# Performance work log

Hardware: AMD Instinct MI355X
Metric: run time of the kernel (lower is better)

The kernel has to match this reference:

```python
import jax, jax.numpy as jnp
import numpy as np

# t2t / fold constants (FuseFormer defaults)
K = 7      # kernel size
S = 3      # stride
P = 3      # padding
H, W = 60, 108          # fold output_size
LH = (H + 2 * P - K) // S + 1   # 20
LW = (W + 2 * P - K) // S + 1   # 36
NVECS = LH * LW                 # 720


def _patch_indices():
    # row[k, i] = k + S*i : row coordinate in the padded image for kernel offset k, window i
    row = jnp.arange(K)[:, None] + S * jnp.arange(LH)[None, :]   # [K, LH]
    col = jnp.arange(K)[:, None] + S * jnp.arange(LW)[None, :]   # [K, LW]
    R = row[:, None, :, None]   # [K,1,LH,1]
    C = col[None, :, None, :]   # [1,K,1,LW] -> broadcast [K,K,LH,LW]
    return R, C


def setup_inputs() -> dict:
    key = jax.random.key(0)
    ks = jax.random.split(key, 5)
    b, n, d, hd = 2, 5760, 512, 1960
    return {
        "x": jax.random.normal(ks[0], (b, n, d), dtype=jnp.float32),
        "W1": jax.random.normal(ks[1], (d, hd), dtype=jnp.float32) * 0.02,
        "b1": jax.random.normal(ks[2], (hd,), dtype=jnp.float32) * 0.02,
        "W2": jax.random.normal(ks[3], (hd, d), dtype=jnp.float32) * 0.02,
        "b2": jax.random.normal(ks[4], (d,), dtype=jnp.float32) * 0.02,
    }


def reference(x, W1, b1, W2, b2):
    b, n, d = x.shape
    h = x @ W1 + b1                      # [b, n, 1960]
    c = h.shape[-1]
    Cch = c // (K * K)                   # 40 channels
    B2 = (b * n) // NVECS                # folded batch

    R, Cc = _patch_indices()

    # fold(x): [B2, C*K*K, L] scatter-add (col2im) into padded image
    hf = h.reshape(B2, NVECS, c).transpose(0, 2, 1)            # [B2, c, L]
    hf = hf.reshape(B2, Cch, K, K, LH, LW)
    padded = jnp.zeros((B2, Cch, H + 2 * P, W + 2 * P), h.dtype)
    padded = padded.at[:, :, R, Cc].add(hf)
    folded = padded[:, :, P:P + H, P:P + W]                    # [B2, C, H, W]

    # fold(ones): overlap-count normalizer (batch-independent, compute once)
    ones6 = jnp.ones((1, 1, K, K, LH, LW), h.dtype)
    npad = jnp.zeros((1, 1, H + 2 * P, W + 2 * P), h.dtype)
    norm = npad.at[:, :, R, Cc].add(ones6)[:, :, P:P + H, P:P + W]

    y = folded / norm                                          # broadcast over channels

    # unfold: im2col gather of 7x7 patches
    ypad = jnp.pad(y, ((0, 0), (0, 0), (P, P), (P, P)))
    patches = ypad[:, :, R, Cc]                                # [B2, C, K, K, LH, LW]
    uf = patches.reshape(B2, c, NVECS).transpose(0, 2, 1).reshape(b, n, c)

    # conv2: ReLU -> (dropout=identity at eval) -> Linear -> (dropout)
    out = jnp.maximum(uf, 0) @ W2 + b2                         # [b, n, d]
    return out
```

## Files before the change

### kernel.cpp

```cpp
#include <hip/hip_runtime.h>
#include <hip/hip_bf16.h>

#define M_ROWS   11520
#define D_IN     512
#define HD       1960
#define HDP      2048
#define CPAD     52
#define K2       2080
#define B2C      16
#define NVECS    720
#define LH       20
#define LW       36
#define HH       60
#define WW       108
#define CCH      40

using bf16x8 = __attribute__((ext_vector_type(8))) short;
using f32x4  = __attribute__((ext_vector_type(4))) float;
using f4     = __attribute__((ext_vector_type(4))) float;
using su4    = __attribute__((ext_vector_type(4))) unsigned short;

__device__ __forceinline__ float bf2f(unsigned short u) {
    unsigned int x = ((unsigned int)u) << 16;
    return __builtin_bit_cast(float, x);
}
__device__ __forceinline__ unsigned short f2bf(float f) {
    unsigned int x = __builtin_bit_cast(unsigned int, f);
    unsigned int r = (x + 0x7fffu + ((x >> 16) & 1u)) >> 16;
    return (unsigned short)r;
}

__device__ __forceinline__ void gl_lds16(const unsigned short* g, unsigned short* l) {
    __builtin_amdgcn_global_load_lds(
        (const __attribute__((address_space(1))) unsigned int*)g,
        (__attribute__((address_space(3))) unsigned int*)l, 16, 0, 0);
}

__global__ __launch_bounds__(256) void prep(
    const float* __restrict__ x, const float* __restrict__ W1, const float* __restrict__ W2,
    unsigned short* __restrict__ xb, unsigned short* __restrict__ w1t,
    unsigned short* __restrict__ w2t)
{
    __shared__ unsigned short tile[32][33];
    int b = blockIdx.x, t = threadIdx.x;
    if (b < 5760) {
        int i = b * 256 + t;
        f4 v = ((const f4*)x)[i];
        su4 o;
        o.x = f2bf(v.x); o.y = f2bf(v.y); o.z = f2bf(v.z); o.w = f2bf(v.w);
        ((su4*)xb)[i] = o;
        return;
    }
    int tx = t & 31, ty = t >> 5;
    if (b < 6784) {
        int blk = b - 5760;
        int kt = blk & 15, nt = blk >> 4;
        int k0 = kt * 32, n0 = nt * 32;
#pragma unroll
        for (int p = 0; p < 4; p++) {
            int k = k0 + ty + p * 8;
            int n = n0 + tx;
            tile[ty + p * 8][tx] = (n < HD) ? f2bf(W1[k * HD + n]) : (unsigned short)0;
        }
        __syncthreads();
#pragma unroll
        for (int p = 0; p < 4; p++) {
            int n = n0 + ty + p * 8;
            int k = k0 + tx;
            w1t[n * 512 + k] = tile[tx][ty + p * 8];
        }
    } else {
        int blk = b - 6784;
        int kt = blk % 62, nt = blk / 62;
        int k0 = kt * 32, n0 = nt * 32;
        if (kt == 0) {
            for (int i = t; i < 32 * CCH * 3; i += 256) {
                int nn = n0 + (i & 31);
                int cc = (i >> 5) / 3, p = (i >> 5) % 3;
                w2t[nn * K2 + cc * CPAD + 49 + p] = 0;
            }
        }
#pragma unroll
        for (int p = 0; p < 4; p++) {
            int k = k0 + ty + p * 8;
            int n = n0 + tx;
            tile[ty + p * 8][tx] = (k < HD) ? f2bf(W2[k * 512 + n]) : (unsigned short)0;
        }
        __syncthreads();
#pragma unroll
        for (int p = 0; p < 4; p++) {
            int n = n0 + ty + p * 8;
            int k = k0 + tx;
            if (k < HD) {
                int cch = k / 49, kk = k - cch * 49;
                w2t[n * K2 + cch * CPAD + kk] = tile[tx][ty + p * 8];
            }
        }
    }
}

__global__ __launch_bounds__(512) void gemm1_blk(
    const unsigned short* __restrict__ A,
    const unsigned short* __restrict__ Bt,
    const float* __restrict__ bias,
    unsigned short* __restrict__ h_blk)
{
    __shared__ unsigned short sA[3 * 128 * 32];
    __shared__ unsigned short sB[3 * 128 * 32];
    const int lda = D_IN, ldb = D_IN;
    const int NT = D_IN / 32;

    int g = (blockIdx.x & 7) * 180 + (blockIdx.x >> 3);
    int bx = g & 15, by = g >> 4;
    int t    = threadIdx.x;
    int w    = t >> 6;
    int lane = t & 63;
    int quad = lane >> 4;
    int l16  = lane & 15;
    int row0 = by * 128, col0 = bx * 128;
    int wr = (w >> 2) * 64;
    int wc = (w & 3) * 32;

    int srow = t >> 2;
    int qb = ((t & 3) - ((srow >> 1) & 3)) & 3;
    const unsigned short* Ag = A  + (size_t)(row0 + srow) * lda + qb * 8;
    const unsigned short* Bg = Bt + (size_t)(col0 + srow) * ldb + qb * 8;
    unsigned short* lA = sA + t * 8;
    unsigned short* lB = sB + t * 8;

    int xq = (quad + ((l16 >> 1) & 3)) & 3;

    f32x4 acc[4][2] = {};

    gl_lds16(Ag, lA);
    gl_lds16(Bg, lB);
    gl_lds16(Ag + 32, lA + 4096);
    gl_lds16(Bg + 32, lB + 4096);

#pragma unroll
    for (int it = 0; it < NT; ++it) {
        const int cur = it % 3;
        if (it + 2 < NT) {
            const int nslot = (it + 2) % 3;
            const int k0n = (it + 2) * 32;
            gl_lds16(Ag + k0n, lA + nslot * 4096);
            gl_lds16(Bg + k0n, lB + nslot * 4096);
            asm volatile("s_waitcnt vmcnt(4)" ::: "memory");
        } else if (it + 1 < NT) {
            asm volatile("s_waitcnt vmcnt(2)" ::: "memory");
        } else {
            asm volatile("s_waitcnt vmcnt(0)" ::: "memory");
        }
        __builtin_amdgcn_s_barrier();
        asm volatile("" ::: "memory");

        const unsigned short* bA = sA + cur * 4096;
        const unsigned short* bB = sB + cur * 4096;

        bf16x8 a[4], bfr[2];
#pragma unroll
        for (int i = 0; i < 4; i++)
            a[i] = *(const bf16x8*)(bA + (wr + i * 16 + l16) * 32 + xq * 8);
#pragma unroll
        for (int j = 0; j < 2; j++)
            bfr[j] = *(const bf16x8*)(bB + (wc + j * 16 + l16) * 32 + xq * 8);
#pragma unroll
        for (int i = 0; i < 4; i++)
#pragma unroll
            for (int j = 0; j < 2; j++)
                acc[i][j] = __builtin_amdgcn_mfma_f32_16x16x32_bf16(a[i], bfr[j], acc[i][j], 0, 0, 0);
        asm volatile("" ::: "memory");
        __builtin_amdgcn_s_barrier();
        asm volatile("" ::: "memory");
    }

    int rowterm[16];
#pragma unroll
    for (int i = 0; i < 4; i++)
#pragma unroll
        for (int r = 0; r < 4; r++) {
            int row = row0 + wr + i * 16 + quad * 4 + r;
            int bb = row / NVECS;
            int sp = row - bb * NVECS;
            rowterm[i * 4 + r] = bb * (CCH * NVECS * CPAD) + sp * CPAD;
        }

#pragma unroll
    for (int j = 0; j < 2; j++) {
        int col = col0 + wc + j * 16 + l16;
        if (col < HD) {
            int cch = col / 49, kk = col - cch * 49;
            int colterm = cch * (NVECS * CPAD) + kk;
            float bv = bias[col];
#pragma unroll
            for (int i = 0; i < 4; i++)
#pragma unroll
                for (int r = 0; r < 4; r++)
                    h_blk[(size_t)rowterm[i * 4 + r] + colterm] = f2bf(acc[i][j][r] + bv);
        }
    }

    int cch0 = col0 / 49;
    int cch1 = (col0 + 127) / 49; if (cch1 > CCH - 1) cch1 = CCH - 1;
    int ncch = cch1 - cch0 + 1;
    if (wc == 0 && l16 < 3 * ncch) {
        int c = l16 / 3, p = l16 - c * 3;
        int padcol = (cch0 + c) * (NVECS * CPAD) + 49 + p;
#pragma unroll
        for (int i = 0; i < 4; i++)
#pragma unroll
            for (int r = 0; r < 4; r++)
                h_blk[(size_t)rowterm[i * 4 + r] + padcol] = 0;
    }
}

__global__ __launch_bounds__(256) void fold_unfold(
    const unsigned short* __restrict__ h_blk,
    unsigned short* __restrict__ uf)
{
    __shared__ unsigned short h_lds[12 * 36 * CPAD];
    __shared__ unsigned short y_lds[33 * WW];
    int bid  = blockIdx.x;
    int half = bid & 1;
    int cch  = (bid >> 1) % CCH;
    int b2   = bid / (CCH * 2);
    int tid  = threadIdx.x;

    int lh_base = half ? 8 : 0;
    int y0 = half ? 27 : 0;
    int ny = half ? 33 : 31;

    const su4* hsrc = (const su4*)(h_blk +
        ((size_t)(b2 * CCH + cch) * NVECS + lh_base * 36) * CPAD);
    su4* hd = (su4*)h_lds;
    for (int i = tid; i < 12 * 36 * CPAD / 4; i += 256)
        hd[i] = hsrc[i];
    __syncthreads();

    if (tid < 216) {
        int c  = tid % 108;
        int rr = tid / 108;
        int cp  = c + 3;
        int q2  = cp / 3, rem2 = cp - q2 * 3;
        bool cv0 = (q2 <= 35);
        bool cv2 = (rem2 == 0) & (q2 >= 2);
        int n2  = 1 + (int)cv0 + (int)cv2;
        float rn2 = (n2 == 3) ? (1.0f / 3.0f) : (n2 == 2 ? 0.5f : 1.0f);
        int ca0 = q2 * CPAD + rem2;
        int ca1 = (q2 - 1) * CPAD + rem2 + 3;
        int ca2 = (q2 - 2) * CPAD + rem2 + 6;
        for (; rr < ny; rr += 2) {
            int r  = y0 + rr;
            int rp = r + 3;
            int q1 = rp / 3, rem1 = rp - q1 * 3;
            bool rv0 = (q1 <= 19);
            bool rv2 = (rem1 == 0) & (q1 >= 2);
            int n1 = 1 + (int)rv0 + (int)rv2;
            float rn1 = (n1 == 3) ? (1.0f / 3.0f) : (n1 == 2 ? 0.5f : 1.0f);
            int ra0 = (q1 - lh_base) * (36 * CPAD) + rem1 * 7;
            int ra1 = ra0 - 36 * CPAD + 21;
            int ra2 = ra0 - 2 * (36 * CPAD) + 42;
            float s = 0.0f;
#define FT(vr, ra, vc, ca) {                                   \
            bool vv = (vr) & (vc);                             \
            int ad = vv ? ((ra) + (ca)) : 0;                   \
            float val = bf2f(h_lds[ad]);                       \
            s += vv ? val : 0.0f; }
            FT(rv0,  ra0, cv0,  ca0)
            FT(rv0,  ra0, true, ca1)
            FT(rv0,  ra0, cv2,  ca2)
            FT(true, ra1, cv0,  ca0)
            FT(true, ra1, true, ca1)
            FT(true, ra1, cv2,  ca2)
            FT(rv2,  ra2, cv0,  ca0)
            FT(rv2,  ra2, true, ca1)
            FT(rv2,  ra2, cv2,  ca2)
#undef FT
            y_lds[rr * WW + c] = f2bf(fmaxf(s * rn1 * rn2, 0.0f));
        }
    }
    __syncthreads();

    if (tid < 247) {
        int q  = tid % 13;
        int ri = tid / 13;
        int j0 = q * 4;
        int lh0 = 10 * half;
        int k1c[4], k2c[4];
        bool jv[4];
#pragma unroll
        for (int e = 0; e < 4; e++) {
            int j = j0 + e;
            jv[e] = (j < 49);
            int k1 = j / 7;
            k1c[e] = k1;
            k2c[e] = j - k1 * 7;
        }
        int lh = lh0, lw = ri;
        for (int rcur = ri; rcur < 360; rcur += 19) {
            int rb = 3 * lh - 3, cb = 3 * lw - 3;
            su4 o;
#pragma unroll
            for (int e = 0; e < 4; e++) {
                unsigned short val = 0;
                if (jv[e]) {
                    int r = rb + k1c[e], cc = cb + k2c[e];
                    if ((unsigned)r < (unsigned)HH && (unsigned)cc < (unsigned)WW)
                        val = y_lds[(r - y0) * WW + cc];
                }
                ((unsigned short*)&o)[e] = val;
            }
            int row = b2 * NVECS + lh * 36 + lw;
            *(su4*)(uf + (size_t)row * K2 + cch * CPAD + j0) = o;
            lw += 19;
            if (lw >= 36) { lw -= 36; lh++; }
        }
    }
}

__global__ __launch_bounds__(512) void gemm2(
    const unsigned short* __restrict__ A,
    const unsigned short* __restrict__ Bt,
    const float* __restrict__ bias,
    float* __restrict__ C)
{
    __shared__ unsigned short sA[3 * 128 * 32];
    __shared__ unsigned short sB[3 * 64 * 32];
    const int lda = K2, ldb = K2, ldc = D_IN;
    const int NT = K2 / 32;

    int g = (blockIdx.x & 7) * 90 + (blockIdx.x >> 3);
    int bx = g & 7, by = g >> 3;
    int t    = threadIdx.x;
    int w    = t >> 6;
    int lane = t & 63;
    int quad = lane >> 4;
    int l16  = lane & 15;
    int row0 = by * 128, col0 = bx * 64;
    int wr = (w >> 1) * 32;
    int wc = (w & 1) * 32;

    bool stager = (t < 256);
    int srow  = t >> 2;
    int srowB = srow & 63;
    int qb  = ((t & 3) - ((srow  >> 1) & 3)) & 3;
    int qbB = ((t & 3) - ((srowB >> 1) & 3)) & 3;
    const unsigned short* Ag = A  + (size_t)(row0 + srow)  * lda + qb  * 8;
    const unsigned short* Bg = Bt + (size_t)(col0 + srowB) * ldb + qbB * 8;
    unsigned short* lA = sA + t * 8;
    unsigned short* lB = sB + t * 8;

    int xq = (quad + ((l16 >> 1) & 3)) & 3;

    f32x4 acc[2][2] = {};

    gl_lds16(Ag, lA);
    if (stager) gl_lds16(Bg, lB);
    gl_lds16(Ag + 32, lA + 4096);
    if (stager) gl_lds16(Bg + 32, lB + 2048);

    for (int it = 0; it < NT; ++it) {
        const int cur = it % 3;
        if (it + 2 < NT) {
            const int nslot = (it + 2) % 3;
            const int k0n = (it + 2) * 32;
            gl_lds16(Ag + k0n, lA + nslot * 4096);
            if (stager) {
                gl_lds16(Bg + k0n, lB + nslot * 2048);
                asm volatile("s_waitcnt vmcnt(4)" ::: "memory");
            } else {
                asm volatile("s_waitcnt vmcnt(2)" ::: "memory");
            }
        } else if (it + 1 < NT) {
            if (stager) asm volatile("s_waitcnt vmcnt(2)" ::: "memory");
            else        asm volatile("s_waitcnt vmcnt(1)" ::: "memory");
        } else {
            asm volatile("s_waitcnt vmcnt(0)" ::: "memory");
        }
        __builtin_amdgcn_s_barrier();
        asm volatile("" ::: "memory");

        const unsigned short* bA = sA + cur * 4096;
        const unsigned short* bB = sB + cur * 2048;

        bf16x8 a[2], bfr[2];
#pragma unroll
        for (int i = 0; i < 2; i++)
            a[i] = *(const bf16x8*)(bA + (wr + i * 16 + l16) * 32 + xq * 8);
#pragma unroll
        for (int j = 0; j < 2; j++)
            bfr[j] = *(const bf16x8*)(bB + (wc + j * 16 + l16) * 32 + xq * 8);
#pragma unroll
        for (int i = 0; i < 2; i++)
#pragma unroll
            for (int j = 0; j < 2; j++)
                acc[i][j] = __builtin_amdgcn_mfma_f32_16x16x32_bf16(a[i], bfr[j], acc[i][j], 0, 0, 0);
        asm volatile("" ::: "memory");
        __builtin_amdgcn_s_barrier();
        asm volatile("" ::: "memory");
    }

#pragma unroll
    for (int j = 0; j < 2; j++) {
        int col = col0 + wc + j * 16 + l16;
        float bv = bias[col];
#pragma unroll
        for (int i = 0; i < 2; i++) {
            int rbase = row0 + wr + i * 16 + quad * 4;
#pragma unroll
            for (int r = 0; r < 4; r++)
                C[(size_t)(rbase + r) * ldc + col] = acc[i][j][r] + bv;
        }
    }
}

extern "C" void kernel_launch(void* const* d_in, const int* in_sizes, int n_in,
                              void* d_out, int out_size, void* d_ws, size_t ws_size,
                              hipStream_t stream) {
    const float* x   = (const float*)d_in[0];
    const float* W1  = (const float*)d_in[1];
    const float* b1  = (const float*)d_in[2];
    const float* W2  = (const float*)d_in[3];
    const float* b2f = (const float*)d_in[4];
    float* out = (float*)d_out;

    unsigned short* ws    = (unsigned short*)d_ws;
    unsigned short* xb    = ws;
    unsigned short* h_blk = xb + (size_t)M_ROWS * D_IN;
    unsigned short* uf    = h_blk + (size_t)M_ROWS * K2;
    unsigned short* w1t   = uf + (size_t)M_ROWS * K2;
    unsigned short* w2t   = w1t + (size_t)HDP * D_IN;

    hipLaunchKernelGGL(prep, dim3(7776), dim3(256), 0, stream, x, W1, W2, xb, w1t, w2t);

    hipLaunchKernelGGL(gemm1_blk, dim3((M_ROWS / 128) * (HDP / 128)), dim3(512), 0, stream,
                       xb, w1t, b1, h_blk);

    hipLaunchKernelGGL(fold_unfold, dim3(B2C * CCH * 2), dim3(256), 0, stream, h_blk, uf);

    hipLaunchKernelGGL(gemm2, dim3((M_ROWS / 128) * (D_IN / 64)), dim3(512), 0, stream,
                       uf, w2t, b2f, out);
}
```

Baseline: 212.0 us.

## Pad gemm2 K to 2112 and use 64-wide double-buffered K steps

Pads the unfolded activation and transposed W2 row stride from 2080 to 2112 and zero-fills the extra columns in prep and fold_unfold. This lets gemm2 process 64 K-elements per iteration with two LDS buffers instead of 32 per iteration with three. The aim is to halve the number of barriers and loop iterations in gemm2. The cost is a small amount of extra MFMA work and memory traffic on the zero padding, less prefetch depth, and extra zero-store work.

Result: faster. 199.2 us (-6.0%).

```diff
diff --git a/kernel.cpp b/kernel.cpp
--- a/kernel.cpp
+++ b/kernel.cpp
@@ -7,6 +7,7 @@
 #define HDP      2048
 #define CPAD     52
 #define K2       2080
+#define K2P      2112
 #define B2C      16
 #define NVECS    720
 #define LH       20
@@ -77,7 +78,12 @@
             for (int i = t; i < 32 * CCH * 3; i += 256) {
                 int nn = n0 + (i & 31);
                 int cc = (i >> 5) / 3, p = (i >> 5) % 3;
-                w2t[nn * K2 + cc * CPAD + 49 + p] = 0;
+                w2t[nn * K2P + cc * CPAD + 49 + p] = 0;
+            }
+            if (t < 256) {
+                su4 z = {};
+                int nn = n0 + (t >> 3), e = t & 7;
+                *(su4*)(w2t + (size_t)nn * K2P + 2080 + e * 4) = z;
             }
         }
 #pragma unroll
@@ -93,7 +99,7 @@
             int k = k0 + tx;
             if (k < HD) {
                 int cch = k / 49, kk = k - cch * 49;
-                w2t[n * K2 + cch * CPAD + kk] = tile[tx][ty + p * 8];
+                w2t[n * K2P + cch * CPAD + kk] = tile[tx][ty + p * 8];
             }
         }
     }
@@ -311,9 +317,18 @@
                 ((unsigned short*)&o)[e] = val;
             }
             int row = b2 * NVECS + lh * 36 + lw;
-            *(su4*)(uf + (size_t)row * K2 + cch * CPAD + j0) = o;
+            *(su4*)(uf + (size_t)row * K2P + cch * CPAD + j0) = o;
             lw += 19;
             if (lw >= 36) { lw -= 36; lh++; }
+        }
+    }
+
+    if (cch == 0) {
+        su4 z = {};
+        size_t base = (size_t)(b2 * NVECS + (10 * half) * 36) * K2P + 2080;
+        for (int i = tid; i < 360 * 8; i += 256) {
+            int rr = i >> 3, e = i & 7;
+            *(su4*)(uf + base + (size_t)rr * K2P + e * 4) = z;
         }
     }
 }
@@ -324,10 +339,10 @@
     const float* __restrict__ bias,
     float* __restrict__ C)
 {
-    __shared__ unsigned short sA[3 * 128 * 32];
-    __shared__ unsigned short sB[3 * 64 * 32];
-    const int lda = K2, ldb = K2, ldc = D_IN;
-    const int NT = K2 / 32;
+    __shared__ unsigned short sA[2 * 2 * 128 * 32];
+    __shared__ unsigned short sB[2 * 2 * 64 * 32];
+    const int lda = K2P, ldb = K2P, ldc = D_IN;
+    const int NT = K2P / 64;
 
     int g = (blockIdx.x & 7) * 90 + (blockIdx.x >> 3);
     int bx = g & 7, by = g >> 3;
@@ -354,47 +369,50 @@
 
     f32x4 acc[2][2] = {};
 
-    gl_lds16(Ag, lA);
-    if (stager) gl_lds16(Bg, lB);
+    gl_lds16(Ag,      lA);
     gl_lds16(Ag + 32, lA + 4096);
-    if (stager) gl_lds16(Bg + 32, lB + 2048);
+    if (stager) {
+        gl_lds16(Bg,      lB);
+        gl_lds16(Bg + 32, lB + 2048);
+    }
 
     for (int it = 0; it < NT; ++it) {
-        const int cur = it % 3;
-        if (it + 2 < NT) {
-            const int nslot = (it + 2) % 3;
-            const int k0n = (it + 2) * 32;
-            gl_lds16(Ag + k0n, lA + nslot * 4096);
+        const int cur = it & 1, nxt = cur ^ 1;
+        if (it + 1 < NT) {
+            const int k0n = (it + 1) * 64;
+            gl_lds16(Ag + k0n,      lA + nxt * 8192);
+            gl_lds16(Ag + k0n + 32, lA + nxt * 8192 + 4096);
             if (stager) {
-                gl_lds16(Bg + k0n, lB + nslot * 2048);
+                gl_lds16(Bg + k0n,      lB + nxt * 4096);
+                gl_lds16(Bg + k0n + 32, lB + nxt * 4096 + 2048);
                 asm volatile("s_waitcnt vmcnt(4)" ::: "memory");
             } else {
                 asm volatile("s_waitcnt vmcnt(2)" ::: "memory");
             }
-        } else if (it + 1 < NT) {
-            if (stager) asm volatile("s_waitcnt vmcnt(2)" ::: "memory");
-            else        asm volatile("s_waitcnt vmcnt(1)" ::: "memory");
         } else {
             asm volatile("s_waitcnt vmcnt(0)" ::: "memory");
         }
         __builtin_amdgcn_s_barrier();
         asm volatile("" ::: "memory");
 
-        const unsigned short* bA = sA + cur * 4096;
-        const unsigned short* bB = sB + cur * 2048;
-
-        bf16x8 a[2], bfr[2];
-#pragma unroll
-        for (int i = 0; i < 2; i++)
-            a[i] = *(const bf16x8*)(bA + (wr + i * 16 + l16) * 32 + xq * 8);
-#pragma unroll
-        for (int j = 0; j < 2; j++)
-            bfr[j] = *(const bf16x8*)(bB + (wc + j * 16 + l16) * 32 + xq * 8);
-#pragma unroll
-        for (int i = 0; i < 2; i++)
+        const unsigned short* bA = sA + cur * 8192;
+        const unsigned short* bB = sB + cur * 4096;
+
+#pragma unroll
+        for (int s = 0; s < 2; s++) {
+            bf16x8 a[2], bfr[2];
+#pragma unroll
+            for (int i = 0; i < 2; i++)
+                a[i] = *(const bf16x8*)(bA + s * 4096 + (wr + i * 16 + l16) * 32 + xq * 8);
 #pragma unroll
             for (int j = 0; j < 2; j++)
-                acc[i][j] = __builtin_amdgcn_mfma_f32_16x16x32_bf16(a[i], bfr[j], acc[i][j], 0, 0, 0);
+                bfr[j] = *(const bf16x8*)(bB + s * 2048 + (wc + j * 16 + l16) * 32 + xq * 8);
+#pragma unroll
+            for (int i = 0; i < 2; i++)
+#pragma unroll
+                for (int j = 0; j < 2; j++)
+                    acc[i][j] = __builtin_amdgcn_mfma_f32_16x16x32_bf16(a[i], bfr[j], acc[i][j], 0, 0, 0);
+        }
         asm volatile("" ::: "memory");
         __builtin_amdgcn_s_barrier();
         asm volatile("" ::: "memory");
@@ -428,7 +446,7 @@
     unsigned short* xb    = ws;
     unsigned short* h_blk = xb + (size_t)M_ROWS * D_IN;
     unsigned short* uf    = h_blk + (size_t)M_ROWS * K2;
-    unsigned short* w1t   = uf + (size_t)M_ROWS * K2;
+    unsigned short* w1t   = uf + (size_t)M_ROWS * K2P;
     unsigned short* w2t   = w1t + (size_t)HDP * D_IN;
 
     hipLaunchKernelGGL(prep, dim3(7776), dim3(256), 0, stream, x, W1, W2, xb, w1t, w2t);
```
